# Kernel optimization log

Hardware: AMD Instinct MI355X
Metric: run time of the kernel (lower is better)

## Reference

```python
import jax, jax.numpy as jnp
import numpy as np

N_EXPERTS = 8
D_MODEL = 1024
D_FF = 2048
N_TOKENS = 4096
TOP_K = 2


def _init_expert_weight(key, shape):
    # matches torch init: bound = sqrt(3) * (sqrt(1/3)/sqrt(fan_in)) = 1/sqrt(fan_in)
    fan_in = shape[1]
    bound = 1.0 / np.sqrt(fan_in)
    return jax.random.uniform(key, shape, dtype=jnp.float32, minval=-bound, maxval=bound)


def setup_inputs() -> dict:
    key = jax.random.key(0)
    k_x, k_idx, k_w, k1, k2, k3 = jax.random.split(key, 6)
    x = jax.random.normal(k_x, (N_TOKENS, D_MODEL), dtype=jnp.float32)
    expert_indices = jax.random.randint(k_idx, (N_TOKENS, TOP_K), 0, N_EXPERTS)
    expert_weights = jax.random.uniform(k_w, (N_TOKENS, TOP_K), dtype=jnp.float32)
    w1 = _init_expert_weight(k1, (N_EXPERTS, D_MODEL, D_FF))
    w2 = _init_expert_weight(k2, (N_EXPERTS, D_MODEL, D_FF))
    w3 = _init_expert_weight(k3, (N_EXPERTS, D_FF, D_MODEL))
    return {"x": x, "expert_indices": expert_indices, "expert_weights": expert_weights,
            "w1": w1, "w2": w2, "w3": w3}


def reference(x, expert_indices, expert_weights, w1, w2, w3):
    # SwiGLU per expert, computed densely over all (token, expert) pairs,
    # then the top-k selected expert outputs are gathered and combined.
    # Mathematically identical to the padded-bmm dispatch/combine in the source.
    gate = jax.nn.silu(jnp.einsum('td,edf->tef', x, w1))   # [T, E, F]
    value = jnp.einsum('td,edf->tef', x, w2)               # [T, E, F]
    hidden = gate * value                                  # [T, E, F]
    out_e = jnp.einsum('tef,efd->ted', hidden, w3)         # [T, E, D]
    # gather each token's top-k expert outputs: [T, K, D]
    sel = jnp.take_along_axis(out_e, expert_indices[:, :, None], axis=1)
    return jnp.sum(sel * expert_weights[:, :, None], axis=1)  # [T, D]
```

## Files before the change

kernel.cpp:

```cpp
#include <hip/hip_runtime.h>
#include <hip/hip_bf16.h>

#define N_TOK   4096
#define DM      1024
#define DF      2048
#define NEXP    8
#define NPAIR   (N_TOK * 2)
#define BM      128
#define BN      128
#define BK      32
#define LDK     40

typedef __attribute__((ext_vector_type(8))) short bf16x8;
typedef __attribute__((ext_vector_type(4))) float f32x4;

__device__ __forceinline__ unsigned short to_bf16(float f) {
    unsigned u = __builtin_bit_cast(unsigned, f);
    unsigned r = (u + 0x7FFFu + ((u >> 16) & 1u)) >> 16;
    return (unsigned short)r;
}
__device__ __forceinline__ unsigned pk_bf16(float a, float b) {
    return (unsigned)to_bf16(a) | ((unsigned)to_bf16(b) << 16);
}
__device__ __forceinline__ void gld16(const unsigned short* g, unsigned short* l) {
    __builtin_amdgcn_global_load_lds(
        (const __attribute__((address_space(1))) unsigned int*)(g),
        (__attribute__((address_space(3))) unsigned int*)(l), 16, 0, 0);
}

__global__ void k_count(const int* __restrict__ eidx, int* __restrict__ meta) {
    int i = blockIdx.x * 256 + threadIdx.x;
    if (i < NPAIR) atomicAdd(&meta[eidx[i] & 7], 1);
}
__global__ void k_scan(int* __restrict__ meta) {
    if (threadIdx.x == 0) {
        int off = 0, mt = 0;
        for (int e = 0; e < NEXP; ++e) {
            meta[16 + e] = off; meta[25 + e] = mt;
            int c = meta[e];
            off += c; mt += (c + BM - 1) / BM;
        }
        meta[16 + NEXP] = off; meta[25 + NEXP] = mt; meta[34] = mt;
    }
}
__global__ void k_scatter(const int* __restrict__ eidx, int* __restrict__ meta,
                          int* __restrict__ rows) {
    int i = blockIdx.x * 256 + threadIdx.x;
    if (i < NPAIR) {
        int e = eidx[i] & 7;
        int p = meta[16 + e] + atomicAdd(&meta[8 + e], 1);
        rows[p] = i;
    }
}

__global__ __launch_bounds__(256)
void k_cvt_x(const float* __restrict__ x, unsigned short* __restrict__ xb) {
    int i = (blockIdx.x * 256 + threadIdx.x) * 8;
    float4 v0 = *(const float4*)(x + i);
    float4 v1 = *(const float4*)(x + i + 4);
    uint4 w;
    w.x = pk_bf16(v0.x, v0.y); w.y = pk_bf16(v0.z, v0.w);
    w.z = pk_bf16(v1.x, v1.y); w.w = pk_bf16(v1.z, v1.w);
    *(uint4*)(xb + i) = w;
}

__global__ __launch_bounds__(256)
void k_transpose(const float* __restrict__ src, unsigned short* __restrict__ dst,
                 int K, int F) {
    __shared__ __align__(16) unsigned short tile[64 * 80];
    const int e  = blockIdx.z;
    const int k0 = blockIdx.y * 64;
    const int f0 = blockIdx.x * 64;
    const int t  = threadIdx.x;
    const float* s = src + (size_t)e * K * F;
    unsigned short* d = dst + (size_t)e * K * F;
    const int fi = t & 63;
    const int kg = t >> 6;
    #pragma unroll
    for (int i = 0; i < 16; ++i) {
        int k = kg * 16 + i;
        tile[k * 80 + fi] = to_bf16(s[(size_t)(k0 + k) * F + f0 + fi]);
    }
    __syncthreads();
    const int kc = (t & 7) * 8;
    const int fo = t >> 3;
    #pragma unroll
    for (int j = 0; j < 2; ++j) {
        int f = fo + j * 32;
        unsigned short v[8];
        #pragma unroll
        for (int i = 0; i < 8; ++i) v[i] = tile[(kc + i) * 80 + f];
        uint4 w;
        w.x = (unsigned)v[0] | ((unsigned)v[1] << 16);
        w.y = (unsigned)v[2] | ((unsigned)v[3] << 16);
        w.z = (unsigned)v[4] | ((unsigned)v[5] << 16);
        w.w = (unsigned)v[6] | ((unsigned)v[7] << 16);
        *(uint4*)&d[(size_t)(f0 + f) * K + k0 + kc] = w;
    }
}

__global__ __launch_bounds__(256, 2)
void k_gemm1_bf(const unsigned short* __restrict__ xb,
                const unsigned short* __restrict__ w1t,
                const unsigned short* __restrict__ w2t,
                const int* __restrict__ meta,
                const int* __restrict__ rows,
                unsigned short* __restrict__ H)
{
    __shared__ __align__(16) unsigned short As [2][BM * BK];
    __shared__ __align__(16) unsigned short B1s[2][BN * BK];
    __shared__ __align__(16) unsigned short B2s[2][BN * BK];
    __shared__ int s_tok[BM];

    const int mt = blockIdx.y;
    if (mt >= meta[34]) return;
    int e = 0;
    #pragma unroll
    for (int i = 0; i < NEXP - 1; ++i) if (mt >= meta[25 + i + 1]) e = i + 1;
    const int rowEnd = meta[16 + e + 1];
    const int row0   = meta[16 + e] + (mt - meta[25 + e]) * BM;
    const int f0     = blockIdx.x * BN;
    const int tid    = threadIdx.x;

    if (tid < BM) {
        int gr = row0 + tid;
        s_tok[tid] = (gr < rowEnd) ? (rows[gr] >> 1) : 0;
    }
    __syncthreads();

    const int lane = tid & 63;
    const int wave = tid >> 6;
    const int r0 = wave * 32 + (lane >> 2);
    const int r1 = r0 + 16;
    const int kb = (lane & 3) * 8;
    const unsigned short* a_src0 = xb + (size_t)s_tok[r0] * DM + kb;
    const unsigned short* a_src1 = xb + (size_t)s_tok[r1] * DM + kb;
    const size_t wb = (size_t)e * DM * DF;
    const unsigned short* b1_src0 = w1t + wb + (size_t)(f0 + r0) * DM + kb;
    const unsigned short* b1_src1 = w1t + wb + (size_t)(f0 + r1) * DM + kb;
    const unsigned short* b2_src0 = w2t + wb + (size_t)(f0 + r0) * DM + kb;
    const unsigned short* b2_src1 = w2t + wb + (size_t)(f0 + r1) * DM + kb;

    f32x4 accg[4][4], accv[4][4];
    #pragma unroll
    for (int i = 0; i < 4; ++i)
        #pragma unroll
        for (int j = 0; j < 4; ++j) { accg[i][j] = (f32x4)0.f; accv[i][j] = (f32x4)0.f; }

    const int wm = (wave >> 1) * 64;
    const int wn = (wave & 1) * 64;
    const int am = lane & 15;
    const int ak = (lane >> 4) * 8;

    auto stage = [&](int bi, int k0) {
        unsigned short* A0 = &As [bi][wave * 1024];
        unsigned short* B1 = &B1s[bi][wave * 1024];
        unsigned short* B2 = &B2s[bi][wave * 1024];
        gld16(a_src0  + k0, A0);
        gld16(a_src1  + k0, A0 + 512);
        gld16(b1_src0 + k0, B1);
        gld16(b1_src1 + k0, B1 + 512);
        gld16(b2_src0 + k0, B2);
        gld16(b2_src1 + k0, B2 + 512);
    };
    auto compute = [&](int bi) {
        bf16x8 a[4], b1[4], b2[4];
        #pragma unroll
        for (int mi = 0; mi < 4; ++mi) a[mi] = *(const bf16x8*)&As[bi][(wm + mi * 16 + am) * BK + ak];
        #pragma unroll
        for (int ni = 0; ni < 4; ++ni) {
            b1[ni] = *(const bf16x8*)&B1s[bi][(wn + ni * 16 + am) * BK + ak];
            b2[ni] = *(const bf16x8*)&B2s[bi][(wn + ni * 16 + am) * BK + ak];
        }
        #pragma unroll
        for (int mi = 0; mi < 4; ++mi)
            #pragma unroll
            for (int ni = 0; ni < 4; ++ni) {
                accg[mi][ni] = __builtin_amdgcn_mfma_f32_16x16x32_bf16(a[mi], b1[ni], accg[mi][ni], 0, 0, 0);
                accv[mi][ni] = __builtin_amdgcn_mfma_f32_16x16x32_bf16(a[mi], b2[ni], accv[mi][ni], 0, 0, 0);
            }
    };

    stage(0, 0);
    int cur = 0;
    for (int t = 0; t < DM / BK - 1; ++t) {
        stage(cur ^ 1, (t + 1) * BK);
        asm volatile("s_waitcnt vmcnt(6)" ::: "memory");
        __builtin_amdgcn_s_barrier();
        __builtin_amdgcn_sched_barrier(0);
        compute(cur);
        __builtin_amdgcn_sched_barrier(0);
        __builtin_amdgcn_s_barrier();
        cur ^= 1;
    }
    asm volatile("s_waitcnt vmcnt(0)" ::: "memory");
    __builtin_amdgcn_s_barrier();
    __builtin_amdgcn_sched_barrier(0);
    compute(cur);

    const int cn = lane & 15;
    const int cq = (lane >> 4) * 4;
    #pragma unroll
    for (int mi = 0; mi < 4; ++mi) {
        #pragma unroll
        for (int r = 0; r < 4; ++r) {
            const int row = wm + mi * 16 + cq + r;
            const int gr  = row0 + row;
            if (gr < rowEnd) {
                unsigned short* dst = H + (size_t)gr * DF + f0 + wn;
                #pragma unroll
                for (int ni = 0; ni < 4; ++ni) {
                    float g = accg[mi][ni][r];
                    float v = accv[mi][ni][r];
                    float h = (g * v) / (1.f + __expf(-g));
                    dst[ni * 16 + cn] = to_bf16(h);
                }
            }
        }
    }
}

__global__ __launch_bounds__(256, 2)
void k_gemm2_bf(const unsigned short* __restrict__ H,
                const unsigned short* __restrict__ w3t,
                const int* __restrict__ meta,
                const int* __restrict__ rows,
                const float* __restrict__ ew,
                float* __restrict__ out)
{
    __shared__ __align__(16) unsigned short As[2][BM * BK];
    __shared__ __align__(16) unsigned short Bs[2][BN * BK];
    __shared__ int   s_tok[BM];
    __shared__ float s_w[BM];

    const int mt = blockIdx.y;
    if (mt >= meta[34]) return;
    int e = 0;
    #pragma unroll
    for (int i = 0; i < NEXP - 1; ++i) if (mt >= meta[25 + i + 1]) e = i + 1;
    const int rowEnd = meta[16 + e + 1];
    const int row0   = meta[16 + e] + (mt - meta[25 + e]) * BM;
    const int d0     = blockIdx.x * BN;
    const int tid    = threadIdx.x;

    if (tid < BM) {
        int gr = row0 + tid;
        if (gr < rowEnd) { int pr = rows[gr]; s_tok[tid] = pr >> 1; s_w[tid] = ew[pr]; }
        else             { s_tok[tid] = 0;    s_w[tid] = 0.f; }
    }
    __syncthreads();

    const int lane = tid & 63;
    const int wave = tid >> 6;
    const int r0 = wave * 32 + (lane >> 2);
    const int r1 = r0 + 16;
    const int kb = (lane & 3) * 8;
    int gr0 = row0 + r0; if (gr0 > NPAIR - 1) gr0 = NPAIR - 1;
    int gr1 = row0 + r1; if (gr1 > NPAIR - 1) gr1 = NPAIR - 1;
    const unsigned short* a_src0 = H + (size_t)gr0 * DF + kb;
    const unsigned short* a_src1 = H + (size_t)gr1 * DF + kb;
    const size_t wb = (size_t)e * DM * DF;
    const unsigned short* b_src0 = w3t + wb + (size_t)(d0 + r0) * DF + kb;
    const unsigned short* b_src1 = w3t + wb + (size_t)(d0 + r1) * DF + kb;

    f32x4 acc[4][4];
    #pragma unroll
    for (int i = 0; i < 4; ++i)
        #pragma unroll
        for (int j = 0; j < 4; ++j) acc[i][j] = (f32x4)0.f;

    const int wm = (wave >> 1) * 64;
    const int wn = (wave & 1) * 64;
    const int am = lane & 15;
    const int ak = (lane >> 4) * 8;

    auto stage = [&](int bi, int k0) {
        unsigned short* A0 = &As[bi][wave * 1024];
        unsigned short* B0 = &Bs[bi][wave * 1024];
        gld16(a_src0 + k0, A0);
        gld16(a_src1 + k0, A0 + 512);
        gld16(b_src0 + k0, B0);
        gld16(b_src1 + k0, B0 + 512);
    };
    auto compute = [&](int bi) {
        bf16x8 a[4], b[4];
        #pragma unroll
        for (int mi = 0; mi < 4; ++mi) a[mi] = *(const bf16x8*)&As[bi][(wm + mi * 16 + am) * BK + ak];
        #pragma unroll
        for (int ni = 0; ni < 4; ++ni) b[ni] = *(const bf16x8*)&Bs[bi][(wn + ni * 16 + am) * BK + ak];
        #pragma unroll
        for (int mi = 0; mi < 4; ++mi)
            #pragma unroll
            for (int ni = 0; ni < 4; ++ni)
                acc[mi][ni] = __builtin_amdgcn_mfma_f32_16x16x32_bf16(a[mi], b[ni], acc[mi][ni], 0, 0, 0);
    };

    stage(0, 0);
    int cur = 0;
    for (int t = 0; t < DF / BK - 1; ++t) {
        stage(cur ^ 1, (t + 1) * BK);
        asm volatile("s_waitcnt vmcnt(4)" ::: "memory");
        __builtin_amdgcn_s_barrier();
        __builtin_amdgcn_sched_barrier(0);
        compute(cur);
        __builtin_amdgcn_sched_barrier(0);
        __builtin_amdgcn_s_barrier();
        cur ^= 1;
    }
    asm volatile("s_waitcnt vmcnt(0)" ::: "memory");
    __builtin_amdgcn_s_barrier();
    __builtin_amdgcn_sched_barrier(0);
    compute(cur);

    const int cn = lane & 15;
    const int cq = (lane >> 4) * 4;
    #pragma unroll
    for (int mi = 0; mi < 4; ++mi) {
        #pragma unroll
        for (int r = 0; r < 4; ++r) {
            const int row = wm + mi * 16 + cq + r;
            const int gr  = row0 + row;
            if (gr < rowEnd) {
                const int   tok = s_tok[row];
                const float wgt = s_w[row];
                float* dst = out + (size_t)tok * DM + d0 + wn;
                #pragma unroll
                for (int ni = 0; ni < 4; ++ni)
                    atomicAdd(&dst[ni * 16 + cn], wgt * acc[mi][ni][r]);
            }
        }
    }
}

__global__ __launch_bounds__(256, 2)
void k_gemm1(const float* __restrict__ x, const float* __restrict__ w1,
             const float* __restrict__ w2, const int* __restrict__ meta,
             const int* __restrict__ rows, unsigned short* __restrict__ H)
{
    __shared__ unsigned short As[BM][LDK];
    __shared__ unsigned short B1s[BN][LDK];
    __shared__ unsigned short B2s[BN][LDK];
    __shared__ int s_tok[BM];
    const int mt = blockIdx.y;
    if (mt >= meta[34]) return;
    int e = 0;
    #pragma unroll
    for (int i = 0; i < NEXP - 1; ++i) if (mt >= meta[25 + i + 1]) e = i + 1;
    const int rowEnd = meta[16 + e + 1];
    const int row0   = meta[16 + e] + (mt - meta[25 + e]) * BM;
    const int f0     = blockIdx.x * BN;
    const int tid    = threadIdx.x;
    if (tid < BM) {
        int gr = row0 + tid;
        s_tok[tid] = (gr < rowEnd) ? (rows[gr] >> 1) : -1;
    }
    __syncthreads();
    const int ar = tid >> 1;
    const int ah = (tid & 1) * 16;
    const int a_tok = s_tok[ar];
    const float* a_src = x + (size_t)(a_tok < 0 ? 0 : a_tok) * DM + ah;
    const int bn_ = tid & 127;
    const int bk_ = (tid >> 7) * 16;
    const float* b1_src = w1 + (size_t)e * DM * DF + (size_t)bk_ * DF + f0 + bn_;
    const float* b2_src = w2 + (size_t)e * DM * DF + (size_t)bk_ * DF + f0 + bn_;
    f32x4 accg[4][4], accv[4][4];
    #pragma unroll
    for (int i = 0; i < 4; ++i)
        #pragma unroll
        for (int j = 0; j < 4; ++j) { accg[i][j] = (f32x4)0.f; accv[i][j] = (f32x4)0.f; }
    const int lane = tid & 63;
    const int wave = tid >> 6;
    const int wm = (wave >> 1) * 64;
    const int wn = (wave & 1) * 64;
    const int am = lane & 15;
    const int ak = (lane >> 4) * 8;
    for (int k0 = 0; k0 < DM; k0 += BK) {
        {
            const float* p = a_src + k0;
            #pragma unroll
            for (int jj = 0; jj < 4; ++jj) {
                float4 v;
                if (a_tok < 0) { v.x = v.y = v.z = v.w = 0.f; }
                else           { v = *(const float4*)(p + jj * 4); }
                uint2 w;
                w.x = pk_bf16(v.x, v.y); w.y = pk_bf16(v.z, v.w);
                *(uint2*)&As[ar][ah + jj * 4] = w;
            }
        }
        {
            const float* p1 = b1_src + (size_t)k0 * DF;
            const float* p2 = b2_src + (size_t)k0 * DF;
            #pragma unroll
            for (int c = 0; c < 2; ++c) {
                float v[8];
                #pragma unroll
                for (int j = 0; j < 8; ++j) v[j] = p1[(size_t)(c * 8 + j) * DF];
                uint4 w;
                w.x = pk_bf16(v[0], v[1]); w.y = pk_bf16(v[2], v[3]);
                w.z = pk_bf16(v[4], v[5]); w.w = pk_bf16(v[6], v[7]);
                *(uint4*)&B1s[bn_][bk_ + c * 8] = w;
            }
            #pragma unroll
            for (int c = 0; c < 2; ++c) {
                float v[8];
                #pragma unroll
                for (int j = 0; j < 8; ++j) v[j] = p2[(size_t)(c * 8 + j) * DF];
                uint4 w;
                w.x = pk_bf16(v[0], v[1]); w.y = pk_bf16(v[2], v[3]);
                w.z = pk_bf16(v[4], v[5]); w.w = pk_bf16(v[6], v[7]);
                *(uint4*)&B2s[bn_][bk_ + c * 8] = w;
            }
        }
        __syncthreads();
        bf16x8 a[4], b1[4], b2[4];
        #pragma unroll
        for (int mi = 0; mi < 4; ++mi) a[mi] = *(const bf16x8*)&As[wm + mi * 16 + am][ak];
        #pragma unroll
        for (int ni = 0; ni < 4; ++ni) {
            b1[ni] = *(const bf16x8*)&B1s[wn + ni * 16 + am][ak];
            b2[ni] = *(const bf16x8*)&B2s[wn + ni * 16 + am][ak];
        }
        #pragma unroll
        for (int mi = 0; mi < 4; ++mi)
            #pragma unroll
            for (int ni = 0; ni < 4; ++ni) {
                accg[mi][ni] = __builtin_amdgcn_mfma_f32_16x16x32_bf16(a[mi], b1[ni], accg[mi][ni], 0, 0, 0);
                accv[mi][ni] = __builtin_amdgcn_mfma_f32_16x16x32_bf16(a[mi], b2[ni], accv[mi][ni], 0, 0, 0);
            }
        __syncthreads();
    }
    const int cn = lane & 15;
    const int cq = (lane >> 4) * 4;
    #pragma unroll
    for (int mi = 0; mi < 4; ++mi) {
        #pragma unroll
        for (int r = 0; r < 4; ++r) {
            const int row = wm + mi * 16 + cq + r;
            const int gr  = row0 + row;
            if (gr < rowEnd) {
                unsigned short* dst = H + (size_t)gr * DF + f0 + wn;
                #pragma unroll
                for (int ni = 0; ni < 4; ++ni) {
                    float g = accg[mi][ni][r];
                    float v = accv[mi][ni][r];
                    float h = (g * v) / (1.f + __expf(-g));
                    dst[ni * 16 + cn] = to_bf16(h);
                }
            }
        }
    }
}

__global__ __launch_bounds__(256, 2)
void k_gemm2(const unsigned short* __restrict__ H, const float* __restrict__ w3,
             const int* __restrict__ meta, const int* __restrict__ rows,
             const float* __restrict__ ew, float* __restrict__ out)
{
    __shared__ unsigned short As[BM][LDK];
    __shared__ unsigned short Bs[BN][LDK];
    __shared__ int   s_tok[BM];
    __shared__ float s_w[BM];
    const int mt = blockIdx.y;
    if (mt >= meta[34]) return;
    int e = 0;
    #pragma unroll
    for (int i = 0; i < NEXP - 1; ++i) if (mt >= meta[25 + i + 1]) e = i + 1;
    const int rowEnd = meta[16 + e + 1];
    const int row0   = meta[16 + e] + (mt - meta[25 + e]) * BM;
    const int d0     = blockIdx.x * BN;
    const int tid    = threadIdx.x;
    if (tid < BM) {
        int gr = row0 + tid;
        if (gr < rowEnd) { int pr = rows[gr]; s_tok[tid] = pr >> 1; s_w[tid] = ew[pr]; }
        else             { s_tok[tid] = 0;    s_w[tid] = 0.f; }
    }
    __syncthreads();
    const int ar = tid >> 1;
    const int ah = (tid & 1) * 16;
    int a_row = row0 + ar; if (a_row >= NPAIR) a_row = NPAIR - 1;
    const unsigned short* a_src = H + (size_t)a_row * DF + ah;
    const int bn_ = tid & 127;
    const int bk_ = (tid >> 7) * 16;
    const float* b_src = w3 + (size_t)e * DF * DM + (size_t)bk_ * DM + d0 + bn_;
    f32x4 acc[4][4];
    #pragma unroll
    for (int i = 0; i < 4; ++i)
        #pragma unroll
        for (int j = 0; j < 4; ++j) acc[i][j] = (f32x4)0.f;
    const int lane = tid & 63;
    const int wave = tid >> 6;
    const int wm = (wave >> 1) * 64;
    const int wn = (wave & 1) * 64;
    const int am = lane & 15;
    const int ak = (lane >> 4) * 8;
    for (int k0 = 0; k0 < DF; k0 += BK) {
        *(uint4*)&As[ar][ah]     = *(const uint4*)(a_src + k0);
        *(uint4*)&As[ar][ah + 8] = *(const uint4*)(a_src + k0 + 8);
        {
            const float* p = b_src + (size_t)k0 * DM;
            #pragma unroll
            for (int c = 0; c < 2; ++c) {
                float v[8];
                #pragma unroll
                for (int j = 0; j < 8; ++j) v[j] = p[(size_t)(c * 8 + j) * DM];
                uint4 w;
                w.x = pk_bf16(v[0], v[1]); w.y = pk_bf16(v[2], v[3]);
                w.z = pk_bf16(v[4], v[5]); w.w = pk_bf16(v[6], v[7]);
                *(uint4*)&Bs[bn_][bk_ + c * 8] = w;
            }
        }
        __syncthreads();
        bf16x8 a[4], b[4];
        #pragma unroll
        for (int mi = 0; mi < 4; ++mi) a[mi] = *(const bf16x8*)&As[wm + mi * 16 + am][ak];
        #pragma unroll
        for (int ni = 0; ni < 4; ++ni) b[ni] = *(const bf16x8*)&Bs[wn + ni * 16 + am][ak];
        #pragma unroll
        for (int mi = 0; mi < 4; ++mi)
            #pragma unroll
            for (int ni = 0; ni < 4; ++ni)
                acc[mi][ni] = __builtin_amdgcn_mfma_f32_16x16x32_bf16(a[mi], b[ni], acc[mi][ni], 0, 0, 0);
        __syncthreads();
    }
    const int cn = lane & 15;
    const int cq = (lane >> 4) * 4;
    #pragma unroll
    for (int mi = 0; mi < 4; ++mi) {
        #pragma unroll
        for (int r = 0; r < 4; ++r) {
            const int row = wm + mi * 16 + cq + r;
            const int gr  = row0 + row;
            if (gr < rowEnd) {
                const int   tok = s_tok[row];
                const float wgt = s_w[row];
                float* dst = out + (size_t)tok * DM + d0 + wn;
                #pragma unroll
                for (int ni = 0; ni < 4; ++ni)
                    atomicAdd(&dst[ni * 16 + cn], wgt * acc[mi][ni][r]);
            }
        }
    }
}

__global__ __launch_bounds__(256)
void k_fallback(const float* __restrict__ x, const int* __restrict__ eidx,
                const float* __restrict__ ew, const float* __restrict__ w1,
                const float* __restrict__ w2, const float* __restrict__ w3,
                float* __restrict__ out)
{
    __shared__ float xs[DM];
    __shared__ float hs[DF];
    const int pair = blockIdx.x;
    const int t = pair >> 1;
    const int e = eidx[pair] & 7;
    const float wgt = ew[pair];
    const int tid = threadIdx.x;
    for (int i = tid; i < DM; i += 256) xs[i] = x[(size_t)t * DM + i];
    __syncthreads();
    for (int f = tid; f < DF; f += 256) {
        const float* c1 = w1 + (size_t)e * DM * DF + f;
        const float* c2 = w2 + (size_t)e * DM * DF + f;
        float g = 0.f, v = 0.f;
        for (int d = 0; d < DM; ++d) {
            float xv = xs[d];
            g += xv * c1[(size_t)d * DF];
            v += xv * c2[(size_t)d * DF];
        }
        hs[f] = (g * v) / (1.f + __expf(-g));
    }
    __syncthreads();
    for (int d = tid; d < DM; d += 256) {
        const float* c3 = w3 + (size_t)e * DF * DM + d;
        float o = 0.f;
        for (int f = 0; f < DF; ++f) o += hs[f] * c3[(size_t)f * DM];
        atomicAdd(&out[(size_t)t * DM + d], wgt * o);
    }
}

extern "C" void kernel_launch(void* const* d_in, const int* in_sizes, int n_in,
                              void* d_out, int out_size, void* d_ws, size_t ws_size,
                              hipStream_t stream)
{
    const float* x  = (const float*)d_in[0];
    const int*   ei = (const int*)  d_in[1];
    const float* ew = (const float*)d_in[2];
    const float* w1 = (const float*)d_in[3];
    const float* w2 = (const float*)d_in[4];
    const float* w3 = (const float*)d_in[5];
    float* out = (float*)d_out;

    (void)hipMemsetAsync(d_out, 0, (size_t)out_size * sizeof(float), stream);

    const size_t SZ_H  = (size_t)NPAIR * DF * 2;
    const size_t SZ_XB = (size_t)N_TOK * DM * 2;
    const size_t SZ_W  = (size_t)NEXP * DM * DF * 2;
    const size_t OFF_H  = 65536;
    const size_t OFF_XB = OFF_H + SZ_H;
    const size_t OFF_W1 = OFF_XB + SZ_XB;
    const size_t OFF_W2 = OFF_W1 + SZ_W;
    const size_t OFF_W3 = OFF_W2 + SZ_W;
    const size_t NEED_BIG   = OFF_W3 + SZ_W;
    const size_t NEED_SMALL = OFF_H + SZ_H;

    if (ws_size < NEED_SMALL) {
        k_fallback<<<NPAIR, 256, 0, stream>>>(x, ei, ew, w1, w2, w3, out);
        return;
    }

    int* meta = (int*)d_ws;
    int* rows = meta + 64;
    unsigned short* H = (unsigned short*)((char*)d_ws + OFF_H);

    (void)hipMemsetAsync(d_ws, 0, 64, stream);
    k_count  <<<NPAIR / 256, 256, 0, stream>>>(ei, meta);
    k_scan   <<<1, 64, 0, stream>>>(meta);
    k_scatter<<<NPAIR / 256, 256, 0, stream>>>(ei, meta, rows);

    if (ws_size >= NEED_BIG) {
        unsigned short* xb  = (unsigned short*)((char*)d_ws + OFF_XB);
        unsigned short* w1t = (unsigned short*)((char*)d_ws + OFF_W1);
        unsigned short* w2t = (unsigned short*)((char*)d_ws + OFF_W2);
        unsigned short* w3t = (unsigned short*)((char*)d_ws + OFF_W3);
        k_cvt_x<<<(N_TOK * DM) / 2048, 256, 0, stream>>>(x, xb);
        k_transpose<<<dim3(DF / 64, DM / 64, NEXP), 256, 0, stream>>>(w1, w1t, DM, DF);
        k_transpose<<<dim3(DF / 64, DM / 64, NEXP), 256, 0, stream>>>(w2, w2t, DM, DF);
        k_transpose<<<dim3(DM / 64, DF / 64, NEXP), 256, 0, stream>>>(w3, w3t, DF, DM);
        k_gemm1_bf<<<dim3(DF / BN, NPAIR / BM + NEXP), 256, 0, stream>>>(xb, w1t, w2t, meta, rows, H);
        k_gemm2_bf<<<dim3(DM / BN, NPAIR / BM + NEXP), 256, 0, stream>>>(H, w3t, meta, rows, ew, out);
    } else {
        k_gemm1<<<dim3(DF / BN, NPAIR / BM + NEXP), 256, 0, stream>>>(x, w1, w2, meta, rows, H);
        k_gemm2<<<dim3(DM / BN, NPAIR / BM + NEXP), 256, 0, stream>>>(H, w3, meta, rows, ew, out);
    }
}
```

Measured before the change: 495.4 us.

## Enlarge MoE GEMM tiles to 256x128x64 with swizzled LDS and split-K

Both grouped GEMMs move to 512-thread blocks with 256-row M tiles and a K step of 64. LDS tiles get an XOR swizzle to avoid bank conflicts, and the main loop is interleaved in half-steps with barriers and s_setprio around MFMA bursts. The second GEMM also splits K in two over the z grid dimension, relying on the existing atomic accumulation into the output. The fp32 fallback GEMM kernels are removed. The aim is more reuse per loaded tile and better overlap, at the cost of more padding waste on per-expert row tiles and a larger LDS footprint per block.

After: 535.4 us. 8.1% more time.

```diff
diff --git a/kernel.cpp b/kernel.cpp
--- a/kernel.cpp
+++ b/kernel.cpp
@@ -6,10 +6,9 @@
 #define DF      2048
 #define NEXP    8
 #define NPAIR   (N_TOK * 2)
-#define BM      128
-#define BN      128
-#define BK      32
-#define LDK     40
+#define BMT     256
+#define BNT     128
+#define BKT     64
 
 typedef __attribute__((ext_vector_type(8))) short bf16x8;
 typedef __attribute__((ext_vector_type(4))) float f32x4;
@@ -38,7 +37,7 @@
         for (int e = 0; e < NEXP; ++e) {
             meta[16 + e] = off; meta[25 + e] = mt;
             int c = meta[e];
-            off += c; mt += (c + BM - 1) / BM;
+            off += c; mt += (c + BMT - 1) / BMT;
         }
         meta[16 + NEXP] = off; meta[25 + NEXP] = mt; meta[34] = mt;
     }
@@ -99,7 +98,7 @@
     }
 }
 
-__global__ __launch_bounds__(256, 2)
+__global__ __launch_bounds__(512, 2)
 void k_gemm1_bf(const unsigned short* __restrict__ xb,
                 const unsigned short* __restrict__ w1t,
                 const unsigned short* __restrict__ w2t,
@@ -107,10 +106,8 @@
                 const int* __restrict__ rows,
                 unsigned short* __restrict__ H)
 {
-    __shared__ __align__(16) unsigned short As [2][BM * BK];
-    __shared__ __align__(16) unsigned short B1s[2][BN * BK];
-    __shared__ __align__(16) unsigned short B2s[2][BN * BK];
-    __shared__ int s_tok[BM];
+    __shared__ __align__(16) unsigned short L[2][32768];
+    __shared__ int s_tok[BMT];
 
     const int mt = blockIdx.y;
     if (mt >= meta[34]) return;
@@ -118,28 +115,30 @@
     #pragma unroll
     for (int i = 0; i < NEXP - 1; ++i) if (mt >= meta[25 + i + 1]) e = i + 1;
     const int rowEnd = meta[16 + e + 1];
-    const int row0   = meta[16 + e] + (mt - meta[25 + e]) * BM;
-    const int f0     = blockIdx.x * BN;
+    const int row0   = meta[16 + e] + (mt - meta[25 + e]) * BMT;
+    const int f0     = blockIdx.x * BNT;
     const int tid    = threadIdx.x;
 
-    if (tid < BM) {
+    if (tid < BMT) {
         int gr = row0 + tid;
         s_tok[tid] = (gr < rowEnd) ? (rows[gr] >> 1) : 0;
     }
     __syncthreads();
 
     const int lane = tid & 63;
-    const int wave = tid >> 6;
-    const int r0 = wave * 32 + (lane >> 2);
-    const int r1 = r0 + 16;
-    const int kb = (lane & 3) * 8;
-    const unsigned short* a_src0 = xb + (size_t)s_tok[r0] * DM + kb;
-    const unsigned short* a_src1 = xb + (size_t)s_tok[r1] * DM + kb;
+    const int wid  = tid >> 6;
+    const int sr  = wid * 8 + (lane >> 3);
+    const int swz = ((lane & 7) ^ ((lane >> 3) & 7)) * 8;
     const size_t wb = (size_t)e * DM * DF;
-    const unsigned short* b1_src0 = w1t + wb + (size_t)(f0 + r0) * DM + kb;
-    const unsigned short* b1_src1 = w1t + wb + (size_t)(f0 + r1) * DM + kb;
-    const unsigned short* b2_src0 = w2t + wb + (size_t)(f0 + r0) * DM + kb;
-    const unsigned short* b2_src1 = w2t + wb + (size_t)(f0 + r1) * DM + kb;
+
+    const unsigned short* p0 = xb + (size_t)s_tok[       sr] * DM + swz;
+    const unsigned short* p1 = xb + (size_t)s_tok[ 64 +  sr] * DM + swz;
+    const unsigned short* p2 = xb + (size_t)s_tok[128 +  sr] * DM + swz;
+    const unsigned short* p3 = xb + (size_t)s_tok[192 +  sr] * DM + swz;
+    const unsigned short* p4 = w1t + wb + (size_t)(f0 +      sr) * DM + swz;
+    const unsigned short* p5 = w1t + wb + (size_t)(f0 + 64 + sr) * DM + swz;
+    const unsigned short* p6 = w2t + wb + (size_t)(f0 +      sr) * DM + swz;
+    const unsigned short* p7 = w2t + wb + (size_t)(f0 + 64 + sr) * DM + swz;
 
     f32x4 accg[4][4], accv[4][4];
     #pragma unroll
@@ -147,56 +146,85 @@
         #pragma unroll
         for (int j = 0; j < 4; ++j) { accg[i][j] = (f32x4)0.f; accv[i][j] = (f32x4)0.f; }
 
-    const int wm = (wave >> 1) * 64;
-    const int wn = (wave & 1) * 64;
-    const int am = lane & 15;
-    const int ak = (lane >> 4) * 8;
-
-    auto stage = [&](int bi, int k0) {
-        unsigned short* A0 = &As [bi][wave * 1024];
-        unsigned short* B1 = &B1s[bi][wave * 1024];
-        unsigned short* B2 = &B2s[bi][wave * 1024];
-        gld16(a_src0  + k0, A0);
-        gld16(a_src1  + k0, A0 + 512);
-        gld16(b1_src0 + k0, B1);
-        gld16(b1_src1 + k0, B1 + 512);
-        gld16(b2_src0 + k0, B2);
-        gld16(b2_src1 + k0, B2 + 512);
+    const int wm  = (wid >> 1) * 64;
+    const int wn  = (wid & 1) * 64;
+    const int am  = lane & 15;
+    const int cb  = lane >> 4;
+    const int key = am & 7;
+    const int axk0 = ((cb    ) ^ key) << 4;
+    const int axk1 = ((cb + 4) ^ key) << 4;
+
+    auto stage = [&](int b, int k0) {
+        unsigned short* base = &L[0][0] + b * 32768 + wid * 512;
+        gld16(p0 + k0, base);
+        gld16(p1 + k0, base + 4096);
+        gld16(p2 + k0, base + 8192);
+        gld16(p3 + k0, base + 12288);
+        gld16(p4 + k0, base + 16384);
+        gld16(p5 + k0, base + 20480);
+        gld16(p6 + k0, base + 24576);
+        gld16(p7 + k0, base + 28672);
     };
-    auto compute = [&](int bi) {
-        bf16x8 a[4], b1[4], b2[4];
-        #pragma unroll
-        for (int mi = 0; mi < 4; ++mi) a[mi] = *(const bf16x8*)&As[bi][(wm + mi * 16 + am) * BK + ak];
-        #pragma unroll
-        for (int ni = 0; ni < 4; ++ni) {
-            b1[ni] = *(const bf16x8*)&B1s[bi][(wn + ni * 16 + am) * BK + ak];
-            b2[ni] = *(const bf16x8*)&B2s[bi][(wn + ni * 16 + am) * BK + ak];
-        }
-        #pragma unroll
-        for (int mi = 0; mi < 4; ++mi)
+
+    stage(0, 0);
+    #pragma unroll 1
+    for (int t = 0; t < DM / BKT; ++t) {
+        const int buf = t & 1;
+        if (t < DM / BKT - 1) {
+            stage(buf ^ 1, (t + 1) * BKT);
+            __builtin_amdgcn_sched_barrier(0);
+            asm volatile("s_waitcnt vmcnt(8)" ::: "memory");
+        } else {
+            asm volatile("s_waitcnt vmcnt(0)" ::: "memory");
+        }
+        __builtin_amdgcn_s_barrier();
+        const char* A  = (const char*)(&L[0][0] + buf * 32768);
+        const char* B1 = A + 32768;
+        const char* B2 = A + 49152;
+        #pragma unroll
+        for (int ks = 0; ks < 2; ++ks) {
+            const int ax = ks ? axk1 : axk0;
+            bf16x8 b1[4], b2[4], a[2];
             #pragma unroll
             for (int ni = 0; ni < 4; ++ni) {
-                accg[mi][ni] = __builtin_amdgcn_mfma_f32_16x16x32_bf16(a[mi], b1[ni], accg[mi][ni], 0, 0, 0);
-                accv[mi][ni] = __builtin_amdgcn_mfma_f32_16x16x32_bf16(a[mi], b2[ni], accv[mi][ni], 0, 0, 0);
+                const int n = wn + ni * 16 + am;
+                b1[ni] = *(const bf16x8*)(B1 + n * 128 + ax);
+                b2[ni] = *(const bf16x8*)(B2 + n * 128 + ax);
             }
-    };
-
-    stage(0, 0);
-    int cur = 0;
-    for (int t = 0; t < DM / BK - 1; ++t) {
-        stage(cur ^ 1, (t + 1) * BK);
-        asm volatile("s_waitcnt vmcnt(6)" ::: "memory");
-        __builtin_amdgcn_s_barrier();
-        __builtin_amdgcn_sched_barrier(0);
-        compute(cur);
-        __builtin_amdgcn_sched_barrier(0);
-        __builtin_amdgcn_s_barrier();
-        cur ^= 1;
-    }
-    asm volatile("s_waitcnt vmcnt(0)" ::: "memory");
-    __builtin_amdgcn_s_barrier();
-    __builtin_amdgcn_sched_barrier(0);
-    compute(cur);
+            #pragma unroll
+            for (int mi = 0; mi < 2; ++mi)
+                a[mi] = *(const bf16x8*)(A + (wm + mi * 16 + am) * 128 + ax);
+            __builtin_amdgcn_sched_barrier(0);
+            __builtin_amdgcn_s_barrier();
+            __builtin_amdgcn_s_setprio(1);
+            #pragma unroll
+            for (int mi = 0; mi < 2; ++mi)
+                #pragma unroll
+                for (int ni = 0; ni < 4; ++ni) {
+                    accg[mi][ni] = __builtin_amdgcn_mfma_f32_16x16x32_bf16(a[mi], b1[ni], accg[mi][ni], 0, 0, 0);
+                    accv[mi][ni] = __builtin_amdgcn_mfma_f32_16x16x32_bf16(a[mi], b2[ni], accv[mi][ni], 0, 0, 0);
+                }
+            __builtin_amdgcn_s_setprio(0);
+            __builtin_amdgcn_sched_barrier(0);
+            __builtin_amdgcn_s_barrier();
+            #pragma unroll
+            for (int mi = 0; mi < 2; ++mi)
+                a[mi] = *(const bf16x8*)(A + (wm + 32 + mi * 16 + am) * 128 + ax);
+            __builtin_amdgcn_sched_barrier(0);
+            __builtin_amdgcn_s_barrier();
+            __builtin_amdgcn_s_setprio(1);
+            #pragma unroll
+            for (int mi = 0; mi < 2; ++mi)
+                #pragma unroll
+                for (int ni = 0; ni < 4; ++ni) {
+                    accg[2 + mi][ni] = __builtin_amdgcn_mfma_f32_16x16x32_bf16(a[mi], b1[ni], accg[2 + mi][ni], 0, 0, 0);
+                    accv[2 + mi][ni] = __builtin_amdgcn_mfma_f32_16x16x32_bf16(a[mi], b2[ni], accv[2 + mi][ni], 0, 0, 0);
+                }
+            __builtin_amdgcn_s_setprio(0);
+            __builtin_amdgcn_sched_barrier(0);
+            __builtin_amdgcn_s_barrier();
+        }
+    }
 
     const int cn = lane & 15;
     const int cq = (lane >> 4) * 4;
@@ -220,7 +248,7 @@
     }
 }
 
-__global__ __launch_bounds__(256, 2)
+__global__ __launch_bounds__(512, 2)
 void k_gemm2_bf(const unsigned short* __restrict__ H,
                 const unsigned short* __restrict__ w3t,
                 const int* __restrict__ meta,
@@ -228,10 +256,9 @@
                 const float* __restrict__ ew,
                 float* __restrict__ out)
 {
-    __shared__ __align__(16) unsigned short As[2][BM * BK];
-    __shared__ __align__(16) unsigned short Bs[2][BN * BK];
-    __shared__ int   s_tok[BM];
-    __shared__ float s_w[BM];
+    __shared__ __align__(16) unsigned short L[2][24576];
+    __shared__ int   s_tok[BMT];
+    __shared__ float s_w[BMT];
 
     const int mt = blockIdx.y;
     if (mt >= meta[34]) return;
@@ -239,11 +266,12 @@
     #pragma unroll
     for (int i = 0; i < NEXP - 1; ++i) if (mt >= meta[25 + i + 1]) e = i + 1;
     const int rowEnd = meta[16 + e + 1];
-    const int row0   = meta[16 + e] + (mt - meta[25 + e]) * BM;
-    const int d0     = blockIdx.x * BN;
+    const int row0   = meta[16 + e] + (mt - meta[25 + e]) * BMT;
+    const int d0     = blockIdx.x * BNT;
+    const int kz     = blockIdx.z * (DF / 2);
     const int tid    = threadIdx.x;
 
-    if (tid < BM) {
+    if (tid < BMT) {
         int gr = row0 + tid;
         if (gr < rowEnd) { int pr = rows[gr]; s_tok[tid] = pr >> 1; s_w[tid] = ew[pr]; }
         else             { s_tok[tid] = 0;    s_w[tid] = 0.f; }
@@ -251,17 +279,21 @@
     __syncthreads();
 
     const int lane = tid & 63;
-    const int wave = tid >> 6;
-    const int r0 = wave * 32 + (lane >> 2);
-    const int r1 = r0 + 16;
-    const int kb = (lane & 3) * 8;
-    int gr0 = row0 + r0; if (gr0 > NPAIR - 1) gr0 = NPAIR - 1;
-    int gr1 = row0 + r1; if (gr1 > NPAIR - 1) gr1 = NPAIR - 1;
-    const unsigned short* a_src0 = H + (size_t)gr0 * DF + kb;
-    const unsigned short* a_src1 = H + (size_t)gr1 * DF + kb;
+    const int wid  = tid >> 6;
+    const int sr   = wid * 8 + (lane >> 3);
+    const int swz  = ((lane & 7) ^ ((lane >> 3) & 7)) * 8;
     const size_t wb = (size_t)e * DM * DF;
-    const unsigned short* b_src0 = w3t + wb + (size_t)(d0 + r0) * DF + kb;
-    const unsigned short* b_src1 = w3t + wb + (size_t)(d0 + r1) * DF + kb;
+
+    int ga0 = row0 +       sr; if (ga0 > NPAIR - 1) ga0 = NPAIR - 1;
+    int ga1 = row0 +  64 + sr; if (ga1 > NPAIR - 1) ga1 = NPAIR - 1;
+    int ga2 = row0 + 128 + sr; if (ga2 > NPAIR - 1) ga2 = NPAIR - 1;
+    int ga3 = row0 + 192 + sr; if (ga3 > NPAIR - 1) ga3 = NPAIR - 1;
+    const unsigned short* p0 = H + (size_t)ga0 * DF + kz + swz;
+    const unsigned short* p1 = H + (size_t)ga1 * DF + kz + swz;
+    const unsigned short* p2 = H + (size_t)ga2 * DF + kz + swz;
+    const unsigned short* p3 = H + (size_t)ga3 * DF + kz + swz;
+    const unsigned short* p4 = w3t + wb + (size_t)(d0 +      sr) * DF + kz + swz;
+    const unsigned short* p5 = w3t + wb + (size_t)(d0 + 64 + sr) * DF + kz + swz;
 
     f32x4 acc[4][4];
     #pragma unroll
@@ -269,259 +301,76 @@
         #pragma unroll
         for (int j = 0; j < 4; ++j) acc[i][j] = (f32x4)0.f;
 
-    const int wm = (wave >> 1) * 64;
-    const int wn = (wave & 1) * 64;
-    const int am = lane & 15;
-    const int ak = (lane >> 4) * 8;
-
-    auto stage = [&](int bi, int k0) {
-        unsigned short* A0 = &As[bi][wave * 1024];
-        unsigned short* B0 = &Bs[bi][wave * 1024];
-        gld16(a_src0 + k0, A0);
-        gld16(a_src1 + k0, A0 + 512);
-        gld16(b_src0 + k0, B0);
-        gld16(b_src1 + k0, B0 + 512);
+    const int wm  = (wid >> 1) * 64;
+    const int wn  = (wid & 1) * 64;
+    const int am  = lane & 15;
+    const int cb  = lane >> 4;
+    const int key = am & 7;
+    const int axk0 = ((cb    ) ^ key) << 4;
+    const int axk1 = ((cb + 4) ^ key) << 4;
+
+    auto stage = [&](int b, int k0) {
+        unsigned short* base = &L[0][0] + b * 24576 + wid * 512;
+        gld16(p0 + k0, base);
+        gld16(p1 + k0, base + 4096);
+        gld16(p2 + k0, base + 8192);
+        gld16(p3 + k0, base + 12288);
+        gld16(p4 + k0, base + 16384);
+        gld16(p5 + k0, base + 20480);
     };
-    auto compute = [&](int bi) {
-        bf16x8 a[4], b[4];
-        #pragma unroll
-        for (int mi = 0; mi < 4; ++mi) a[mi] = *(const bf16x8*)&As[bi][(wm + mi * 16 + am) * BK + ak];
-        #pragma unroll
-        for (int ni = 0; ni < 4; ++ni) b[ni] = *(const bf16x8*)&Bs[bi][(wn + ni * 16 + am) * BK + ak];
-        #pragma unroll
-        for (int mi = 0; mi < 4; ++mi)
+
+    stage(0, 0);
+    #pragma unroll 1
+    for (int t = 0; t < (DF / 2) / BKT; ++t) {
+        const int buf = t & 1;
+        if (t < (DF / 2) / BKT - 1) {
+            stage(buf ^ 1, (t + 1) * BKT);
+            __builtin_amdgcn_sched_barrier(0);
+            asm volatile("s_waitcnt vmcnt(6)" ::: "memory");
+        } else {
+            asm volatile("s_waitcnt vmcnt(0)" ::: "memory");
+        }
+        __builtin_amdgcn_s_barrier();
+        const char* A = (const char*)(&L[0][0] + buf * 24576);
+        const char* B = A + 32768;
+        #pragma unroll
+        for (int ks = 0; ks < 2; ++ks) {
+            const int ax = ks ? axk1 : axk0;
+            bf16x8 b[4], a[2];
             #pragma unroll
             for (int ni = 0; ni < 4; ++ni)
-                acc[mi][ni] = __builtin_amdgcn_mfma_f32_16x16x32_bf16(a[mi], b[ni], acc[mi][ni], 0, 0, 0);
-    };
-
-    stage(0, 0);
-    int cur = 0;
-    for (int t = 0; t < DF / BK - 1; ++t) {
-        stage(cur ^ 1, (t + 1) * BK);
-        asm volatile("s_waitcnt vmcnt(4)" ::: "memory");
-        __builtin_amdgcn_s_barrier();
-        __builtin_amdgcn_sched_barrier(0);
-        compute(cur);
-        __builtin_amdgcn_sched_barrier(0);
-        __builtin_amdgcn_s_barrier();
-        cur ^= 1;
-    }
-    asm volatile("s_waitcnt vmcnt(0)" ::: "memory");
-    __builtin_amdgcn_s_barrier();
-    __builtin_amdgcn_sched_barrier(0);
-    compute(cur);
-
-    const int cn = lane & 15;
-    const int cq = (lane >> 4) * 4;
-    #pragma unroll
-    for (int mi = 0; mi < 4; ++mi) {
-        #pragma unroll
-        for (int r = 0; r < 4; ++r) {
-            const int row = wm + mi * 16 + cq + r;
-            const int gr  = row0 + row;
-            if (gr < rowEnd) {
-                const int   tok = s_tok[row];
-                const float wgt = s_w[row];
-                float* dst = out + (size_t)tok * DM + d0 + wn;
+                b[ni] = *(const bf16x8*)(B + (wn + ni * 16 + am) * 128 + ax);
+            #pragma unroll
+            for (int mi = 0; mi < 2; ++mi)
+                a[mi] = *(const bf16x8*)(A + (wm + mi * 16 + am) * 128 + ax);
+            __builtin_amdgcn_sched_barrier(0);
+            __builtin_amdgcn_s_barrier();
+            __builtin_amdgcn_s_setprio(1);
+            #pragma unroll
+            for (int mi = 0; mi < 2; ++mi)
                 #pragma unroll
                 for (int ni = 0; ni < 4; ++ni)
-                    atomicAdd(&dst[ni * 16 + cn], wgt * acc[mi][ni][r]);
-            }
-        }
-    }
-}
-
-__global__ __launch_bounds__(256, 2)
-void k_gemm1(const float* __restrict__ x, const float* __restrict__ w1,
-             const float* __restrict__ w2, const int* __restrict__ meta,
-             const int* __restrict__ rows, unsigned short* __restrict__ H)
-{
-    __shared__ unsigned short As[BM][LDK];
-    __shared__ unsigned short B1s[BN][LDK];
-    __shared__ unsigned short B2s[BN][LDK];
-    __shared__ int s_tok[BM];
-    const int mt = blockIdx.y;
-    if (mt >= meta[34]) return;
-    int e = 0;
-    #pragma unroll
-    for (int i = 0; i < NEXP - 1; ++i) if (mt >= meta[25 + i + 1]) e = i + 1;
-    const int rowEnd = meta[16 + e + 1];
-    const int row0   = meta[16 + e] + (mt - meta[25 + e]) * BM;
-    const int f0     = blockIdx.x * BN;
-    const int tid    = threadIdx.x;
-    if (tid < BM) {
-        int gr = row0 + tid;
-        s_tok[tid] = (gr < rowEnd) ? (rows[gr] >> 1) : -1;
-    }
-    __syncthreads();
-    const int ar = tid >> 1;
-    const int ah = (tid & 1) * 16;
-    const int a_tok = s_tok[ar];
-    const float* a_src = x + (size_t)(a_tok < 0 ? 0 : a_tok) * DM + ah;
-    const int bn_ = tid & 127;
-    const int bk_ = (tid >> 7) * 16;
-    const float* b1_src = w1 + (size_t)e * DM * DF + (size_t)bk_ * DF + f0 + bn_;
-    const float* b2_src = w2 + (size_t)e * DM * DF + (size_t)bk_ * DF + f0 + bn_;
-    f32x4 accg[4][4], accv[4][4];
-    #pragma unroll
-    for (int i = 0; i < 4; ++i)
-        #pragma unroll
-        for (int j = 0; j < 4; ++j) { accg[i][j] = (f32x4)0.f; accv[i][j] = (f32x4)0.f; }
-    const int lane = tid & 63;
-    const int wave = tid >> 6;
-    const int wm = (wave >> 1) * 64;
-    const int wn = (wave & 1) * 64;
-    const int am = lane & 15;
-    const int ak = (lane >> 4) * 8;
-    for (int k0 = 0; k0 < DM; k0 += BK) {
-        {
-            const float* p = a_src + k0;
-            #pragma unroll
-            for (int jj = 0; jj < 4; ++jj) {
-                float4 v;
-                if (a_tok < 0) { v.x = v.y = v.z = v.w = 0.f; }
-                else           { v = *(const float4*)(p + jj * 4); }
-                uint2 w;
-                w.x = pk_bf16(v.x, v.y); w.y = pk_bf16(v.z, v.w);
-                *(uint2*)&As[ar][ah + jj * 4] = w;
-            }
-        }
-        {
-            const float* p1 = b1_src + (size_t)k0 * DF;
-            const float* p2 = b2_src + (size_t)k0 * DF;
-            #pragma unroll
-            for (int c = 0; c < 2; ++c) {
-                float v[8];
-                #pragma unroll
-                for (int j = 0; j < 8; ++j) v[j] = p1[(size_t)(c * 8 + j) * DF];
-                uint4 w;
-                w.x = pk_bf16(v[0], v[1]); w.y = pk_bf16(v[2], v[3]);
-                w.z = pk_bf16(v[4], v[5]); w.w = pk_bf16(v[6], v[7]);
-                *(uint4*)&B1s[bn_][bk_ + c * 8] = w;
-            }
-            #pragma unroll
-            for (int c = 0; c < 2; ++c) {
-                float v[8];
-                #pragma unroll
-                for (int j = 0; j < 8; ++j) v[j] = p2[(size_t)(c * 8 + j) * DF];
-                uint4 w;
-                w.x = pk_bf16(v[0], v[1]); w.y = pk_bf16(v[2], v[3]);
-                w.z = pk_bf16(v[4], v[5]); w.w = pk_bf16(v[6], v[7]);
-                *(uint4*)&B2s[bn_][bk_ + c * 8] = w;
-            }
-        }
-        __syncthreads();
-        bf16x8 a[4], b1[4], b2[4];
-        #pragma unroll
-        for (int mi = 0; mi < 4; ++mi) a[mi] = *(const bf16x8*)&As[wm + mi * 16 + am][ak];
-        #pragma unroll
-        for (int ni = 0; ni < 4; ++ni) {
-            b1[ni] = *(const bf16x8*)&B1s[wn + ni * 16 + am][ak];
-            b2[ni] = *(const bf16x8*)&B2s[wn + ni * 16 + am][ak];
-        }
-        #pragma unroll
-        for (int mi = 0; mi < 4; ++mi)
-            #pragma unroll
-            for (int ni = 0; ni < 4; ++ni) {
-                accg[mi][ni] = __builtin_amdgcn_mfma_f32_16x16x32_bf16(a[mi], b1[ni], accg[mi][ni], 0, 0, 0);
-                accv[mi][ni] = __builtin_amdgcn_mfma_f32_16x16x32_bf16(a[mi], b2[ni], accv[mi][ni], 0, 0, 0);
-            }
-        __syncthreads();
-    }
-    const int cn = lane & 15;
-    const int cq = (lane >> 4) * 4;
-    #pragma unroll
-    for (int mi = 0; mi < 4; ++mi) {
-        #pragma unroll
-        for (int r = 0; r < 4; ++r) {
-            const int row = wm + mi * 16 + cq + r;
-            const int gr  = row0 + row;
-            if (gr < rowEnd) {
-                unsigned short* dst = H + (size_t)gr * DF + f0 + wn;
-                #pragma unroll
-                for (int ni = 0; ni < 4; ++ni) {
-                    float g = accg[mi][ni][r];
-                    float v = accv[mi][ni][r];
-                    float h = (g * v) / (1.f + __expf(-g));
-                    dst[ni * 16 + cn] = to_bf16(h);
-                }
-            }
-        }
-    }
-}
-
-__global__ __launch_bounds__(256, 2)
-void k_gemm2(const unsigned short* __restrict__ H, const float* __restrict__ w3,
-             const int* __restrict__ meta, const int* __restrict__ rows,
-             const float* __restrict__ ew, float* __restrict__ out)
-{
-    __shared__ unsigned short As[BM][LDK];
-    __shared__ unsigned short Bs[BN][LDK];
-    __shared__ int   s_tok[BM];
-    __shared__ float s_w[BM];
-    const int mt = blockIdx.y;
-    if (mt >= meta[34]) return;
-    int e = 0;
-    #pragma unroll
-    for (int i = 0; i < NEXP - 1; ++i) if (mt >= meta[25 + i + 1]) e = i + 1;
-    const int rowEnd = meta[16 + e + 1];
-    const int row0   = meta[16 + e] + (mt - meta[25 + e]) * BM;
-    const int d0     = blockIdx.x * BN;
-    const int tid    = threadIdx.x;
-    if (tid < BM) {
-        int gr = row0 + tid;
-        if (gr < rowEnd) { int pr = rows[gr]; s_tok[tid] = pr >> 1; s_w[tid] = ew[pr]; }
-        else             { s_tok[tid] = 0;    s_w[tid] = 0.f; }
-    }
-    __syncthreads();
-    const int ar = tid >> 1;
-    const int ah = (tid & 1) * 16;
-    int a_row = row0 + ar; if (a_row >= NPAIR) a_row = NPAIR - 1;
-    const unsigned short* a_src = H + (size_t)a_row * DF + ah;
-    const int bn_ = tid & 127;
-    const int bk_ = (tid >> 7) * 16;
-    const float* b_src = w3 + (size_t)e * DF * DM + (size_t)bk_ * DM + d0 + bn_;
-    f32x4 acc[4][4];
-    #pragma unroll
-    for (int i = 0; i < 4; ++i)
-        #pragma unroll
-        for (int j = 0; j < 4; ++j) acc[i][j] = (f32x4)0.f;
-    const int lane = tid & 63;
-    const int wave = tid >> 6;
-    const int wm = (wave >> 1) * 64;
-    const int wn = (wave & 1) * 64;
-    const int am = lane & 15;
-    const int ak = (lane >> 4) * 8;
-    for (int k0 = 0; k0 < DF; k0 += BK) {
-        *(uint4*)&As[ar][ah]     = *(const uint4*)(a_src + k0);
-        *(uint4*)&As[ar][ah + 8] = *(const uint4*)(a_src + k0 + 8);
-        {
-            const float* p = b_src + (size_t)k0 * DM;
-            #pragma unroll
-            for (int c = 0; c < 2; ++c) {
-                float v[8];
-                #pragma unroll
-                for (int j = 0; j < 8; ++j) v[j] = p[(size_t)(c * 8 + j) * DM];
-                uint4 w;
-                w.x = pk_bf16(v[0], v[1]); w.y = pk_bf16(v[2], v[3]);
-                w.z = pk_bf16(v[4], v[5]); w.w = pk_bf16(v[6], v[7]);
-                *(uint4*)&Bs[bn_][bk_ + c * 8] = w;
-            }
-        }
-        __syncthreads();
-        bf16x8 a[4], b[4];
-        #pragma unroll
-        for (int mi = 0; mi < 4; ++mi) a[mi] = *(const bf16x8*)&As[wm + mi * 16 + am][ak];
-        #pragma unroll
-        for (int ni = 0; ni < 4; ++ni) b[ni] = *(const bf16x8*)&Bs[wn + ni * 16 + am][ak];
-        #pragma unroll
-        for (int mi = 0; mi < 4; ++mi)
-            #pragma unroll
-            for (int ni = 0; ni < 4; ++ni)
-                acc[mi][ni] = __builtin_amdgcn_mfma_f32_16x16x32_bf16(a[mi], b[ni], acc[mi][ni], 0, 0, 0);
-        __syncthreads();
-    }
+                    acc[mi][ni] = __builtin_amdgcn_mfma_f32_16x16x32_bf16(a[mi], b[ni], acc[mi][ni], 0, 0, 0);
+            __builtin_amdgcn_s_setprio(0);
+            __builtin_amdgcn_sched_barrier(0);
+            __builtin_amdgcn_s_barrier();
+            #pragma unroll
+            for (int mi = 0; mi < 2; ++mi)
+                a[mi] = *(const bf16x8*)(A + (wm + 32 + mi * 16 + am) * 128 + ax);
+            __builtin_amdgcn_sched_barrier(0);
+            __builtin_amdgcn_s_barrier();
+            __builtin_amdgcn_s_setprio(1);
+            #pragma unroll
+            for (int mi = 0; mi < 2; ++mi)
+                #pragma unroll
+                for (int ni = 0; ni < 4; ++ni)
+                    acc[2 + mi][ni] = __builtin_amdgcn_mfma_f32_16x16x32_bf16(a[mi], b[ni], acc[2 + mi][ni], 0, 0, 0);
+            __builtin_amdgcn_s_setprio(0);
+            __builtin_amdgcn_sched_barrier(0);
+            __builtin_amdgcn_s_barrier();
+        }
+    }
+
     const int cn = lane & 15;
     const int cq = (lane >> 4) * 4;
     #pragma unroll
@@ -599,36 +448,32 @@
     const size_t OFF_W1 = OFF_XB + SZ_XB;
     const size_t OFF_W2 = OFF_W1 + SZ_W;
     const size_t OFF_W3 = OFF_W2 + SZ_W;
-    const size_t NEED_BIG   = OFF_W3 + SZ_W;
-    const size_t NEED_SMALL = OFF_H + SZ_H;
-
-    if (ws_size < NEED_SMALL) {
+    const size_t NEED_BIG = OFF_W3 + SZ_W;
+
+    if (ws_size < NEED_BIG) {
         k_fallback<<<NPAIR, 256, 0, stream>>>(x, ei, ew, w1, w2, w3, out);
         return;
     }
 
     int* meta = (int*)d_ws;
     int* rows = meta + 64;
-    unsigned short* H = (unsigned short*)((char*)d_ws + OFF_H);
+    unsigned short* H   = (unsigned short*)((char*)d_ws + OFF_H);
+    unsigned short* xb  = (unsigned short*)((char*)d_ws + OFF_XB);
+    unsigned short* w1t = (unsigned short*)((char*)d_ws + OFF_W1);
+    unsigned short* w2t = (unsigned short*)((char*)d_ws + OFF_W2);
+    unsigned short* w3t = (unsigned short*)((char*)d_ws + OFF_W3);
 
     (void)hipMemsetAsync(d_ws, 0, 64, stream);
     k_count  <<<NPAIR / 256, 256, 0, stream>>>(ei, meta);
     k_scan   <<<1, 64, 0, stream>>>(meta);
     k_scatter<<<NPAIR / 256, 256, 0, stream>>>(ei, meta, rows);
 
-    if (ws_size >= NEED_BIG) {
-        unsigned short* xb  = (unsigned short*)((char*)d_ws + OFF_XB);
-        unsigned short* w1t = (unsigned short*)((char*)d_ws + OFF_W1);
-        unsigned short* w2t = (unsigned short*)((char*)d_ws + OFF_W2);
-        unsigned short* w3t = (unsigned short*)((char*)d_ws + OFF_W3);
-        k_cvt_x<<<(N_TOK * DM) / 2048, 256, 0, stream>>>(x, xb);
-        k_transpose<<<dim3(DF / 64, DM / 64, NEXP), 256, 0, stream>>>(w1, w1t, DM, DF);
-        k_transpose<<<dim3(DF / 64, DM / 64, NEXP), 256, 0, stream>>>(w2, w2t, DM, DF);
-        k_transpose<<<dim3(DM / 64, DF / 64, NEXP), 256, 0, stream>>>(w3, w3t, DF, DM);
-        k_gemm1_bf<<<dim3(DF / BN, NPAIR / BM + NEXP), 256, 0, stream>>>(xb, w1t, w2t, meta, rows, H);
-        k_gemm2_bf<<<dim3(DM / BN, NPAIR / BM + NEXP), 256, 0, stream>>>(H, w3t, meta, rows, ew, out);
-    } else {
-        k_gemm1<<<dim3(DF / BN, NPAIR / BM + NEXP), 256, 0, stream>>>(x, w1, w2, meta, rows, H);
-        k_gemm2<<<dim3(DM / BN, NPAIR / BM + NEXP), 256, 0, stream>>>(H, w3, meta, rows, ew, out);
-    }
-}
+    k_cvt_x<<<(N_TOK * DM) / 2048, 256, 0, stream>>>(x, xb);
+    k_transpose<<<dim3(DF / 64, DM / 64, NEXP), 256, 0, stream>>>(w1, w1t, DM, DF);
+    k_transpose<<<dim3(DF / 64, DM / 64, NEXP), 256, 0, stream>>>(w2, w2t, DM, DF);
+    k_transpose<<<dim3(DM / 64, DF / 64, NEXP), 256, 0, stream>>>(w3, w3t, DF, DM);
+
+    const int NMT = NPAIR / BMT + NEXP;
+    k_gemm1_bf<<<dim3(DF / BNT, NMT),    512, 0, stream>>>(xb, w1t, w2t, meta, rows, H);
+    k_gemm2_bf<<<dim3(DM / BNT, NMT, 2), 512, 0, stream>>>(H, w3t, meta, rows, ew, out);
+}
```
